# Kernel optimization log

Hardware: AMD Instinct MI355X
Metric: run time of the kernel (lower is better)

The kernel has to match this reference:

```python
import jax, jax.numpy as jnp
import numpy as np
from jax import lax

IN_DIM = 256
MID = IN_DIM // 2          # 128
NUM_FILTERS = 8
OUT_DIM = 256
EMBED_DIM = 256
BN_EPS = 1e-5


def star_relu(x, scale, bias):
    # StarReLU: s * relu(x)**2 + b
    return scale * jnp.square(jax.nn.relu(x)) + bias


def setup_inputs() -> dict:
    key = jax.random.key(0)
    ks = jax.random.split(key, 12)
    B, H, W = 2, 16, 16
    h, w = 128, 128
    inp = {
        "x": jax.random.normal(ks[0], (B, IN_DIM, H, W), jnp.float32),
        "y": jax.random.normal(ks[1], (B, OUT_DIM, h, w), jnp.float32),
        # feature_fuse: 1x1 conv, depthwise 3x3 conv, BatchNorm (eval-mode stats)
        "conv1_w": jax.random.normal(ks[2], (MID, IN_DIM), jnp.float32) * 0.02,
        "conv1_b": jnp.zeros((MID,), jnp.float32),
        "dw_w": jax.random.normal(ks[3], (MID, 3, 3), jnp.float32) * 0.02,
        "dw_b": jnp.zeros((MID,), jnp.float32),
        "bn_gamma": jnp.ones((MID,), jnp.float32),
        "bn_beta": jnp.zeros((MID,), jnp.float32),
        "bn_mean": jax.random.normal(ks[4], (MID,), jnp.float32) * 0.1,
        "bn_var": jax.random.uniform(ks[5], (MID,), jnp.float32, 0.5, 1.5),
        "sr1_scale": jnp.ones((1,), jnp.float32),
        "sr1_bias": jnp.zeros((1,), jnp.float32),
        # channle_expand 1x1 conv
        "ce_w": jax.random.normal(ks[6], (NUM_FILTERS, MID), jnp.float32) * 0.02,
        "ce_b": jnp.zeros((NUM_FILTERS,), jnp.float32),
        "sr2_scale": jnp.ones((1,), jnp.float32),
        "sr2_bias": jnp.zeros((1,), jnp.float32),
        "W_base": jax.random.normal(ks[7], (OUT_DIM * EMBED_DIM, NUM_FILTERS), jnp.float32) * 0.02,
    }
    return inp


def reference(x, y, conv1_w, conv1_b, dw_w, dw_b, bn_gamma, bn_beta, bn_mean,
              bn_var, sr1_scale, sr1_bias, ce_w, ce_b, sr2_scale, sr2_bias, W_base):
    B, _, fh, fw = x.shape
    b, c, h, w = y.shape
    ph, pw = h // fh, w // fw

    # feature_fuse
    t = jnp.einsum('bchw,oc->bohw', x, conv1_w) + conv1_b[None, :, None, None]
    t = lax.conv_general_dilated(
        t, dw_w[:, None, :, :], (1, 1), ((1, 1), (1, 1)),
        feature_group_count=MID,
        dimension_numbers=('NCHW', 'OIHW', 'NCHW')) + dw_b[None, :, None, None]
    t = bn_gamma[None, :, None, None] * (t - bn_mean[None, :, None, None]) \
        * lax.rsqrt(bn_var + BN_EPS)[None, :, None, None] + bn_beta[None, :, None, None]
    t = star_relu(t, sr1_scale, sr1_bias)

    # channle_expand + act -> per-location filter coefficients [b, F, fh, fw]
    wdec = star_relu(jnp.einsum('bchw,fc->bfhw', t, ce_w) + ce_b[None, :, None, None],
                     sr2_scale, sr2_bias)

    # hypernetwork: [b, E*O, fh, fw], flattened as (embed_dim, out_dim)
    Wd = jnp.einsum('bfhw,ef->behw', wdec, W_base)
    Wd = Wd.reshape(b, EMBED_DIM, OUT_DIM, fh, fw)

    # massive-group 1x1 conv == per-(batch, block) small GEMM over spatial patches
    yb = y.reshape(b, c, fh, ph, fw, pw)
    out = jnp.einsum('beoij,boipjq->beipjq', Wd, yb)  # [b, E, fh, ph, fw, pw]
    return out.reshape(b, EMBED_DIM, h, w)
```

## Files before the change

kernel.cpp:

```cpp
#include <hip/hip_runtime.h>
#include <stdint.h>

typedef unsigned short u16t;
typedef unsigned int   u32t;
typedef _Float16       h16;
typedef __attribute__((ext_vector_type(2))) _Float16 h16x2;
typedef __attribute__((ext_vector_type(8))) short    short8;
typedef __attribute__((ext_vector_type(4))) float    f32x4;

#if defined(__has_builtin)
#if __has_builtin(__builtin_amdgcn_fdot2)
#define HAVE_DOT2 1
#endif
#endif

__device__ __forceinline__ float dot2h(u32t a, u32t b, float c){
#ifdef HAVE_DOT2
  return __builtin_amdgcn_fdot2(__builtin_bit_cast(h16x2, a),
                                __builtin_bit_cast(h16x2, b), c, false);
#else
  h16x2 ha = __builtin_bit_cast(h16x2, a), hb = __builtin_bit_cast(h16x2, b);
  return c + (float)ha[0]*(float)hb[0] + (float)ha[1]*(float)hb[1];
#endif
}

__device__ __forceinline__ float bf2f(u16t h){
  union { u32t u; float f; } c; c.u = ((u32t)h) << 16; return c.f;
}
__device__ __forceinline__ u32t pk2bf(float a, float b){
  u32t ua = __builtin_bit_cast(u32t, a) + 0x8000u;
  u32t ub = __builtin_bit_cast(u32t, b) + 0x8000u;
  return __builtin_amdgcn_perm(ub, ua, 0x07060302u);
}
__device__ __forceinline__ u32t pk2h(float a, float b){
  h16x2 h = { (h16)a, (h16)b };
  return __builtin_bit_cast(u32t, h);
}

template<bool BF>
__device__ __forceinline__ float ldv(const void* p, size_t i){
  if constexpr (BF) return bf2f(((const u16t*)p)[i]);
  else              return ((const float*)p)[i];
}
template<bool BF>
__device__ __forceinline__ void ld8(const void* p, size_t i, float* v){
  if constexpr (BF){
    uint4 u = *(const uint4*)((const u16t*)p + i);
    const u32t a[4] = {u.x, u.y, u.z, u.w};
#pragma unroll
    for (int d = 0; d < 4; ++d){
      v[2*d]   = bf2f((u16t)(a[d] & 0xffffu));
      v[2*d+1] = bf2f((u16t)(a[d] >> 16));
    }
  } else {
    const float4* q = (const float4*)((const float*)p + i);
    float4 A = q[0], B = q[1];
    v[0]=A.x; v[1]=A.y; v[2]=A.z; v[3]=A.w;
    v[4]=B.x; v[5]=B.y; v[6]=B.z; v[7]=B.w;
  }
}
template<bool BF>
__device__ __forceinline__ void ld8pk(const void* p, size_t i, u32t* dst){
  if constexpr (BF){
    uint4 u = *(const uint4*)((const u16t*)p + i);
    dst[0]=u.x; dst[1]=u.y; dst[2]=u.z; dst[3]=u.w;
  } else {
    const float4* q = (const float4*)((const float*)p + i);
    float4 A = q[0], B = q[1];
    dst[0] = pk2bf(A.x, A.y); dst[1] = pk2bf(A.z, A.w);
    dst[2] = pk2bf(B.x, B.y); dst[3] = pk2bf(B.z, B.w);
  }
}

__device__ __forceinline__ bool probe_bf(const void* xv){
  const u16t* p = (const u16t*)xv;
  const int lane = threadIdx.x & 63;
  const u16t h0 = p[lane], h1 = p[lane + 64];
  const int e0 = (h0 >> 7) & 0xff, e1 = (h1 >> 7) & 0xff;
  unsigned long long b0 = __ballot(e0 >= 90 && e0 <= 150);
  unsigned long long b1 = __ballot(e1 >= 90 && e1 <= 150);
  return (__popcll(b0) + __popcll(b1)) >= 104;
}

template<bool BF>
__device__ __forceinline__ void pre12_body(
    const void* x, const void* w, const void* bias,
    const void* dww, const void* dwb,
    const void* bng, const void* bnb, const void* bnm, const void* bnv,
    const void* s1s, const void* s1b, float* t2)
{
  __shared__ float ts[256];
  const int bid = blockIdx.x;
  const int b = bid >> 7, c = bid & 127;
  const int ij = threadIdx.x, i = ij >> 4, j = ij & 15;
  float a0 = ldv<BF>(bias, c);
  const size_t xb = (size_t)b * 65536 + ij;
#pragma unroll 8
  for (int k = 0; k < 256; ++k)
    a0 += ldv<BF>(x, xb + (size_t)k * 256) * ldv<BF>(w, (size_t)c * 256 + k);
  ts[ij] = a0;
  __syncthreads();
  float s = ldv<BF>(dwb, c);
#pragma unroll
  for (int di = 0; di < 3; ++di){
    const int ii = i + di - 1;
    if (ii < 0 || ii > 15) continue;
#pragma unroll
    for (int dj = 0; dj < 3; ++dj){
      const int jj = j + dj - 1;
      if (jj < 0 || jj > 15) continue;
      s += ts[ii * 16 + jj] * ldv<BF>(dww, c * 9 + di * 3 + dj);
    }
  }
  const float v = ldv<BF>(bng, c) * (s - ldv<BF>(bnm, c)) *
                  rsqrtf(ldv<BF>(bnv, c) + 1e-5f) + ldv<BF>(bnb, c);
  const float r = fmaxf(v, 0.0f);
  t2[((size_t)b * 128 + c) * 256 + ij] = ldv<BF>(s1s, 0) * r * r + ldv<BF>(s1b, 0);
}
__global__ __launch_bounds__(256) void k_pre12(
    const void* x, const void* w, const void* bias,
    const void* dww, const void* dwb,
    const void* bng, const void* bnb, const void* bnm, const void* bnv,
    const void* s1s, const void* s1b, float* t2){
  if (probe_bf(x)) pre12_body<true >(x,w,bias,dww,dwb,bng,bnb,bnm,bnv,s1s,s1b,t2);
  else             pre12_body<false>(x,w,bias,dww,dwb,bng,bnb,bnm,bnv,s1s,s1b,t2);
}

template<bool BF>
__device__ __forceinline__ void pre3_body(
    const void* x, const float* t2, const void* cew, const void* ceb,
    const void* s2s, const void* s2b, uint4* wdech)
{
  __shared__ float cs[8][128];
  const int b = blockIdx.x, ij = threadIdx.x;
  for (int t = ij; t < 1024; t += 256) cs[t >> 7][t & 127] = ldv<BF>(cew, t);
  __syncthreads();
  float a[8];
#pragma unroll
  for (int f = 0; f < 8; ++f) a[f] = ldv<BF>(ceb, f);
#pragma unroll 4
  for (int c = 0; c < 128; ++c){
    const float tv = t2[((size_t)b * 128 + c) * 256 + ij];
#pragma unroll
    for (int f = 0; f < 8; ++f) a[f] += tv * cs[f][c];
  }
  const float sc2 = ldv<BF>(s2s, 0), sb2 = ldv<BF>(s2b, 0);
  float o[8];
#pragma unroll
  for (int f = 0; f < 8; ++f){
    const float r = fmaxf(a[f], 0.0f);
    o[f] = sc2 * r * r + sb2;
  }
  wdech[b * 256 + ij] = make_uint4(pk2h(o[0], o[1]), pk2h(o[2], o[3]),
                                   pk2h(o[4], o[5]), pk2h(o[6], o[7]));
}
__global__ __launch_bounds__(256) void k_pre3(
    const void* x, const float* t2, const void* cew, const void* ceb,
    const void* s2s, const void* s2b, uint4* wdech){
  if (probe_bf(x)) pre3_body<true >(x, t2, cew, ceb, s2s, s2b, wdech);
  else             pre3_body<false>(x, t2, cew, ceb, s2s, s2b, wdech);
}

template<bool BF>
__device__ __forceinline__ void prew_body(const void* wb, uint4* wbh2){
  const int t = blockIdx.x * 256 + threadIdx.x;
  const int e = t & 255, o = t >> 8;
  float v[8];
  ld8<BF>(wb, ((size_t)e * 256 + o) * 8, v);
  wbh2[(size_t)o * 256 + e] = make_uint4(pk2h(v[0], v[1]), pk2h(v[2], v[3]),
                                         pk2h(v[4], v[5]), pk2h(v[6], v[7]));
}
__global__ __launch_bounds__(256) void k_prew(const void* x, const void* wb, uint4* wbh2){
  if (probe_bf(x)) prew_body<true >(wb, wbh2);
  else             prew_body<false>(wb, wbh2);
}

template<bool BF>
__device__ __forceinline__ void main_body(
    const void* y, const uint4* wbh2, const uint4* wdech, float* out, u16t* smem)
{
  const int bid = blockIdx.x;
  const int ec  = (bid >> 3) & 1;
  const int gx  = (bid & 7) | ((bid >> 4) << 3);
  const int b   = gx >> 7;
  const int i   = (gx >> 3) & 15;
  const int j0  = (gx & 7) * 2;
  const int tid = threadIdx.x;

  {
    const int o_oct = tid & 31;
    const int p     = (tid >> 5) & 7;
    const int g     = tid >> 8;
    u32t Rp[8][4];
#pragma unroll
    for (int r = 0; r < 8; ++r){
      const size_t idx = (((size_t)(b * 256 + o_oct * 8 + r)) * 128 + (i * 8 + p)) * 128
                       + (j0 + g) * 8;
      ld8pk<BF>(y, idx, Rp[r]);
    }
#pragma unroll
    for (int q = 0; q < 8; ++q){
      const int d = q >> 1, h = q & 1;
      u32t cc[4];
#pragma unroll
      for (int k = 0; k < 4; ++k){
        const u32t lo32 = Rp[2*k][d], hi32 = Rp[2*k+1][d];
        cc[k] = h ? ((lo32 >> 16)     | (hi32 & 0xffff0000u))
                  : ((lo32 & 0xffffu) | (hi32 << 16));
      }
      const int row  = g * 64 + p * 8 + q;
      const int phys = (o_oct + row) & 31;
      *(uint4*)(smem + row * 256 + phys * 8) = make_uint4(cc[0], cc[1], cc[2], cc[3]);
    }
  }

  const int wave = tid >> 6, lane = tid & 63;
  const int l15 = lane & 15, l4 = lane >> 4;
  const int e0  = ec * 128 + wave * 16;

  u32t wdp[2][4];
#pragma unroll
  for (int g = 0; g < 2; ++g){
    const uint4 q = wdech[b * 256 + i * 16 + j0 + g];
    wdp[g][0] = q.x; wdp[g][1] = q.y; wdp[g][2] = q.z; wdp[g][3] = q.w;
  }

  const uint4* wrow = wbh2 + (size_t)(l4 * 8) * 256 + e0 + l15;

  uint4 Wb[2][8];
#pragma unroll
  for (int r = 0; r < 8; ++r) Wb[0][r] = wrow[(size_t)r * 256];

  f32x4 acc[2][4];
#pragma unroll
  for (int g = 0; g < 2; ++g)
#pragma unroll
    for (int nt = 0; nt < 4; ++nt)
      acc[g][nt] = (f32x4){0.f, 0.f, 0.f, 0.f};

  __syncthreads();

#pragma unroll
  for (int ks = 0; ks < 8; ++ks){
    const int cur = ks & 1;
    if (ks < 7){
#pragma unroll
      for (int r = 0; r < 8; ++r)
        Wb[cur ^ 1][r] = wrow[(size_t)((ks + 1) * 32 + r) * 256];
    }
    float s[2][8];
#pragma unroll
    for (int r = 0; r < 8; ++r){
      const uint4 w4 = Wb[cur][r];
#pragma unroll
      for (int g = 0; g < 2; ++g){
        float t = dot2h(w4.x, wdp[g][0], 0.0f);
        t = dot2h(w4.y, wdp[g][1], t);
        t = dot2h(w4.z, wdp[g][2], t);
        s[g][r] = dot2h(w4.w, wdp[g][3], t);
      }
    }
#pragma unroll
    for (int g = 0; g < 2; ++g){
      u32t a4[4];
#pragma unroll
      for (int d = 0; d < 4; ++d) a4[d] = pk2bf(s[g][2*d], s[g][2*d+1]);
      const short8 af = __builtin_bit_cast(short8, *(uint4*)a4);
#pragma unroll
      for (int nt = 0; nt < 4; ++nt){
        const int row  = g * 64 + nt * 16 + l15;
        const int phys = (ks * 4 + l4 + row) & 31;
        const short8 bfr = *(const short8*)(smem + row * 256 + phys * 8);
        acc[g][nt] = __builtin_amdgcn_mfma_f32_16x16x32_bf16(af, bfr, acc[g][nt], 0, 0, 0);
      }
    }
  }

#pragma unroll
  for (int g = 0; g < 2; ++g){
#pragma unroll
    for (int nt = 0; nt < 4; ++nt){
      const int col = nt * 16 + l15;
      const int pp = col >> 3, qq = col & 7;
#pragma unroll
      for (int r = 0; r < 4; ++r){
        const int ee = e0 + l4 * 4 + r;
        const size_t oaddr = ((size_t)(b * 256 + ee) * 128 + (i * 8 + pp)) * 128
                           + (j0 + g) * 8 + qq;
        out[oaddr] = acc[g][nt][r];
      }
    }
  }
}
__global__ __launch_bounds__(512, 4) void k_main(
    const void* x, const void* y, const uint4* wbh2, const uint4* wdech, float* out){
  extern __shared__ __align__(16) u16t smem[];
  if (probe_bf(x)) main_body<true >(y, wbh2, wdech, out, smem);
  else             main_body<false>(y, wbh2, wdech, out, smem);
}

extern "C" void kernel_launch(void* const* d_in, const int* in_sizes, int n_in,
                              void* d_out, int out_size, void* d_ws, size_t ws_size,
                              hipStream_t stream)
{
  float* t2    = (float*)d_ws;
  uint4* wdech = (uint4*)((char*)d_ws + 262144);
  uint4* wbh2  = (uint4*)((char*)d_ws + 270336);

  k_pre12<<<dim3(256), dim3(256), 0, stream>>>(
      d_in[0], d_in[2], d_in[3], d_in[4], d_in[5], d_in[6], d_in[7],
      d_in[8], d_in[9], d_in[10], d_in[11], t2);
  k_pre3<<<dim3(2), dim3(256), 0, stream>>>(
      d_in[0], t2, d_in[12], d_in[13], d_in[14], d_in[15], wdech);
  k_prew<<<dim3(256), dim3(256), 0, stream>>>(d_in[0], d_in[16], wbh2);

  const int lds_bytes = 2 * 64 * 256 * 2;
  hipFuncSetAttribute((const void*)k_main,
                      hipFuncAttributeMaxDynamicSharedMemorySize, lds_bytes);
  k_main<<<dim3(512), dim3(512), lds_bytes, stream>>>(
      d_in[0], d_in[1], wbh2, wdech, (float*)d_out);
}
```

Baseline: 173.6 us.

## Precompute hypernetwork A-fragments before the LDS barrier and write bf16 output

The hypernetwork dot products that build the MFMA A-operands now run before the __syncthreads instead of inside the MFMA loop. They are computed in half-steps of four weight rows, double-buffered, and stored as packed bf16 fragments in registers. This lets the W loads and dot2 math overlap with the cooperative y-tile staging into LDS, and leaves a lean MFMA loop afterward. The cost is a larger register footprint (64 extra VGPRs for the fragments), which may reduce occupancy under the 512x4 launch bound. The output store also writes bf16 when the inputs are bf16, which is a dtype-correctness change.

```diff
diff --git a/kernel.cpp b/kernel.cpp
--- a/kernel.cpp
+++ b/kernel.cpp
@@ -31,6 +31,10 @@
   u32t ua = __builtin_bit_cast(u32t, a) + 0x8000u;
   u32t ub = __builtin_bit_cast(u32t, b) + 0x8000u;
   return __builtin_amdgcn_perm(ub, ua, 0x07060302u);
+}
+__device__ __forceinline__ u16t f2bf(float f){
+  u32t u = __builtin_bit_cast(u32t, f) + 0x8000u;
+  return (u16t)(u >> 16);
 }
 __device__ __forceinline__ u32t pk2h(float a, float b){
   h16x2 h = { (h16)a, (h16)b };
@@ -177,7 +181,7 @@
 
 template<bool BF>
 __device__ __forceinline__ void main_body(
-    const void* y, const uint4* wbh2, const uint4* wdech, float* out, u16t* smem)
+    const void* y, const uint4* wbh2, const uint4* wdech, void* out, u16t* smem)
 {
   const int bid = blockIdx.x;
   const int ec  = (bid >> 3) & 1;
@@ -227,9 +231,40 @@
 
   const uint4* wrow = wbh2 + (size_t)(l4 * 8) * 256 + e0 + l15;
 
-  uint4 Wb[2][8];
-#pragma unroll
-  for (int r = 0; r < 8; ++r) Wb[0][r] = wrow[(size_t)r * 256];
+  u32t afr[8][2][4];
+  uint4 W4[2][4];
+#pragma unroll
+  for (int r = 0; r < 4; ++r) W4[0][r] = wrow[(size_t)r * 256];
+
+#pragma unroll
+  for (int half = 0; half < 16; ++half){
+    const int cur = half & 1;
+    if (half < 15){
+#pragma unroll
+      for (int r = 0; r < 4; ++r)
+        W4[cur ^ 1][r] = wrow[(size_t)(((half + 1) * 4 + r) & 7) * 256
+                              + (size_t)(((half + 1) >> 1)) * 32 * 256];
+    }
+    const int ks = half >> 1, dbase = (half & 1) * 2;
+#pragma unroll
+    for (int pr = 0; pr < 2; ++pr){
+      const uint4 wa = W4[cur][2*pr], wb = W4[cur][2*pr + 1];
+#pragma unroll
+      for (int g = 0; g < 2; ++g){
+        float sa = dot2h(wa.x, wdp[g][0], 0.0f);
+        sa = dot2h(wa.y, wdp[g][1], sa);
+        sa = dot2h(wa.z, wdp[g][2], sa);
+        sa = dot2h(wa.w, wdp[g][3], sa);
+        float sb = dot2h(wb.x, wdp[g][0], 0.0f);
+        sb = dot2h(wb.y, wdp[g][1], sb);
+        sb = dot2h(wb.z, wdp[g][2], sb);
+        sb = dot2h(wb.w, wdp[g][3], sb);
+        afr[ks][g][dbase + pr] = pk2bf(sa, sb);
+      }
+    }
+  }
+
+  __syncthreads();
 
   f32x4 acc[2][4];
 #pragma unroll
@@ -238,34 +273,11 @@
     for (int nt = 0; nt < 4; ++nt)
       acc[g][nt] = (f32x4){0.f, 0.f, 0.f, 0.f};
 
-  __syncthreads();
-
 #pragma unroll
   for (int ks = 0; ks < 8; ++ks){
-    const int cur = ks & 1;
-    if (ks < 7){
-#pragma unroll
-      for (int r = 0; r < 8; ++r)
-        Wb[cur ^ 1][r] = wrow[(size_t)((ks + 1) * 32 + r) * 256];
-    }
-    float s[2][8];
-#pragma unroll
-    for (int r = 0; r < 8; ++r){
-      const uint4 w4 = Wb[cur][r];
-#pragma unroll
-      for (int g = 0; g < 2; ++g){
-        float t = dot2h(w4.x, wdp[g][0], 0.0f);
-        t = dot2h(w4.y, wdp[g][1], t);
-        t = dot2h(w4.z, wdp[g][2], t);
-        s[g][r] = dot2h(w4.w, wdp[g][3], t);
-      }
-    }
 #pragma unroll
     for (int g = 0; g < 2; ++g){
-      u32t a4[4];
-#pragma unroll
-      for (int d = 0; d < 4; ++d) a4[d] = pk2bf(s[g][2*d], s[g][2*d+1]);
-      const short8 af = __builtin_bit_cast(short8, *(uint4*)a4);
+      const short8 af = __builtin_bit_cast(short8, *(uint4*)afr[ks][g]);
 #pragma unroll
       for (int nt = 0; nt < 4; ++nt){
         const int row  = g * 64 + nt * 16 + l15;
@@ -287,13 +299,15 @@
         const int ee = e0 + l4 * 4 + r;
         const size_t oaddr = ((size_t)(b * 256 + ee) * 128 + (i * 8 + pp)) * 128
                            + (j0 + g) * 8 + qq;
-        out[oaddr] = acc[g][nt][r];
+        const float v = acc[g][nt][r];
+        if constexpr (BF) ((u16t*)out)[oaddr] = f2bf(v);
+        else              ((float*)out)[oaddr] = v;
       }
     }
   }
 }
 __global__ __launch_bounds__(512, 4) void k_main(
-    const void* x, const void* y, const uint4* wbh2, const uint4* wdech, float* out){
+    const void* x, const void* y, const uint4* wbh2, const uint4* wdech, void* out){
   extern __shared__ __align__(16) u16t smem[];
   if (probe_bf(x)) main_body<true >(y, wbh2, wdech, out, smem);
   else             main_body<false>(y, wbh2, wdech, out, smem);
@@ -318,5 +332,5 @@
   hipFuncSetAttribute((const void*)k_main,
                       hipFuncAttributeMaxDynamicSharedMemorySize, lds_bytes);
   k_main<<<dim3(512), dim3(512), lds_bytes, stream>>>(
-      d_in[0], d_in[1], wbh2, wdech, (float*)d_out);
-}
+      d_in[0], d_in[1], wbh2, wdech, d_out);
+}
```

After: 269.8 us. 55.4% more time.
